# Kernel optimization log

Measured on AMD Instinct MI355X. Metric: run time of the kernel, lower is better.

Reference implementation:

```python
import jax, jax.numpy as jnp
import numpy as np

N_NODES = 50000
NEG_SLOPE = 0.01  # torch F.leaky_relu default


def setup_inputs() -> dict:
    key = jax.random.key(0)
    k1, k2, k3, k4, k5 = jax.random.split(key, 5)
    N, E, D = N_NODES, 800000, 128
    h = jax.random.normal(k1, (N, D), dtype=jnp.float32)
    src = jax.random.randint(k2, (E,), 0, N, dtype=jnp.int32)
    dst = jnp.sort(jax.random.randint(k3, (E,), 0, N, dtype=jnp.int32))
    # xavier-normal-ish scaling
    W_fc = jax.random.normal(k4, (D, D), dtype=jnp.float32) * np.sqrt(2.0 / (D + D))
    attn_w = jax.random.normal(k5, (1, 2 * D), dtype=jnp.float32) * np.sqrt(2.0 / (2 * D + 1))
    return {"h": h, "src": src, "dst": dst, "W_fc": W_fc, "attn_w": attn_w}


def reference(h, src, dst, W_fc, attn_w):
    N = h.shape[0]
    D = W_fc.shape[0]
    # node projection: z = fc(h)
    z = h @ W_fc.T                                   # [N, D]
    # edge attention: e = leaky_relu(attn_fc(cat(z_src, z_dst)))
    a_l, a_r = attn_w[0, :D], attn_w[0, D:]
    logits_l = z @ a_l                               # [N]
    logits_r = z @ a_r                               # [N]
    e = jax.nn.leaky_relu(logits_l[src] + logits_r[dst], NEG_SLOPE)  # [E]
    # segment softmax over incoming edges of each dst node
    m = jax.ops.segment_max(e, dst, num_segments=N)  # [N], -inf for empty
    m = jnp.where(jnp.isfinite(m), m, 0.0)
    ex = jnp.exp(e - m[dst])                         # [E]
    s = jax.ops.segment_sum(ex, dst, num_segments=N) # [N]
    alpha = ex / s[dst]                              # [E]
    # weighted neighbor aggregation: h_out[v] = sum_u alpha_uv * z_u
    out = jax.ops.segment_sum(alpha[:, None] * z[src], dst, num_segments=N)  # [N, D]
    return out
```

## Files before the change

kernel.cpp:

```cpp
#include <hip/hip_runtime.h>
#include <hip/hip_bf16.h>

#define DD 128
#define NEGS 0.01f

typedef float  f32x4 __attribute__((ext_vector_type(4)));
typedef __bf16 bf16x8 __attribute__((ext_vector_type(8)));
typedef unsigned short us8 __attribute__((ext_vector_type(8)));

__device__ __forceinline__ unsigned short f2bf(float f) {
    unsigned int u = __builtin_bit_cast(unsigned int, f);
    u += 0x7FFFu + ((u >> 16) & 1u);
    return (unsigned short)(u >> 16);
}
__device__ __forceinline__ float sb2f(unsigned int u, int byte) {
    return (float)(int)(signed char)((u >> (byte * 8)) & 0xffu);
}

__global__ __launch_bounds__(256)
void k_gemm(const float* __restrict__ h, const float* __restrict__ W,
            const float* __restrict__ attn, const int* __restrict__ dst,
            int E, int N, int NB,
            signed char* __restrict__ z8, float2* __restrict__ lls,
            float* __restrict__ lrv, int* __restrict__ start)
{
    if (blockIdx.x >= NB) {
        int n = (blockIdx.x - NB) * 256 + threadIdx.x;
        if (n > N) return;
        int lo = 0, hi = E;
        while (lo < hi) {
            int mid = (lo + hi) >> 1;
            if (dst[mid] < n) lo = mid + 1; else hi = mid;
        }
        start[n] = lo;
        return;
    }

    __shared__ unsigned short hs[128 * DD];
    __shared__ unsigned short ws[DD * DD];
    const int tid  = threadIdx.x;
    const int row0 = blockIdx.x * 128;

    {
        const int r = tid >> 4, c = tid & 15;
#pragma unroll
        for (int p = 0; p < DD; p += 16) {
            const int rr = p + r;
            const float* pw = W + (size_t)rr * DD + c * 8;
            float4 a = *(const float4*)pw, b = *(const float4*)(pw + 4);
            us8 v = { f2bf(a.x), f2bf(a.y), f2bf(a.z), f2bf(a.w),
                      f2bf(b.x), f2bf(b.y), f2bf(b.z), f2bf(b.w) };
            *(us8*)(ws + rr * DD + ((c ^ (rr & 15)) * 8)) = v;
        }
    }
    {
        const int r = tid >> 4, c = tid & 15;
#pragma unroll
        for (int p = 0; p < 128; p += 16) {
            const int rr = p + r;
            int gr = row0 + rr; if (gr > N - 1) gr = N - 1;
            const float* ph = h + (size_t)gr * DD + c * 8;
            float4 a = *(const float4*)ph, b = *(const float4*)(ph + 4);
            us8 v = { f2bf(a.x), f2bf(a.y), f2bf(a.z), f2bf(a.w),
                      f2bf(b.x), f2bf(b.y), f2bf(b.z), f2bf(b.w) };
            *(us8*)(hs + rr * DD + ((c ^ (rr & 15)) * 8)) = v;
        }
    }
    __syncthreads();

    const int w    = tid >> 6;
    const int lane = tid & 63;
    const int hl   = lane & 15;
    const int g    = lane >> 4;

    f32x4 acc[2][8];
#pragma unroll
    for (int rt = 0; rt < 2; ++rt)
#pragma unroll
        for (int jt = 0; jt < 8; ++jt) acc[rt][jt] = f32x4{0.f, 0.f, 0.f, 0.f};

#pragma unroll
    for (int kk = 0; kk < DD; kk += 32) {
        const int cb = (kk >> 3) + g;
        const int ra0 = w * 32 + hl;
        const int ra1 = ra0 + 16;
        bf16x8 a0 = *(const bf16x8*)(hs + ra0 * DD + ((cb ^ (ra0 & 15)) * 8));
        bf16x8 a1 = *(const bf16x8*)(hs + ra1 * DD + ((cb ^ (ra1 & 15)) * 8));
#pragma unroll
        for (int jt = 0; jt < 8; ++jt) {
            const int rb = jt * 16 + hl;
            bf16x8 b = *(const bf16x8*)(ws + rb * DD + ((cb ^ (rb & 15)) * 8));
            acc[0][jt] = __builtin_amdgcn_mfma_f32_16x16x32_bf16(a0, b, acc[0][jt], 0, 0, 0);
            acc[1][jt] = __builtin_amdgcn_mfma_f32_16x16x32_bf16(a1, b, acc[1][jt], 0, 0, 0);
        }
    }

    float aLc[8], aRc[8];
#pragma unroll
    for (int jt = 0; jt < 8; ++jt) {
        aLc[jt] = attn[jt * 16 + hl];
        aRc[jt] = attn[DD + jt * 16 + hl];
    }
#pragma unroll
    for (int rt = 0; rt < 2; ++rt) {
#pragma unroll
        for (int reg = 0; reg < 4; ++reg) {
            const int row = row0 + w * 32 + rt * 16 + g * 4 + reg;
            float pl = 0.f, pr = 0.f, am = 0.f;
#pragma unroll
            for (int jt = 0; jt < 8; ++jt) {
                float v = acc[rt][jt][reg];
                pl = fmaf(v, aLc[jt], pl);
                pr = fmaf(v, aRc[jt], pr);
                am = fmaxf(am, fabsf(v));
            }
#pragma unroll
            for (int o = 8; o >= 1; o >>= 1) {
                pl += __shfl_xor(pl, o);
                pr += __shfl_xor(pr, o);
                am = fmaxf(am, __shfl_xor(am, o));
            }
            if (row < N) {
                const float inv_s = (am > 0.f) ? 127.f / am : 0.f;
                if (hl == 0) {
                    lls[row] = make_float2(pl, am * (1.f / 127.f));
                    lrv[row] = pr;
                }
                signed char* zr = z8 + (size_t)row * DD;
#pragma unroll
                for (int jt = 0; jt < 8; ++jt)
                    zr[jt * 16 + hl] =
                        (signed char)__float2int_rn(acc[rt][jt][reg] * inv_s);
            }
        }
    }
}

__global__ __launch_bounds__(256)
void k_out(const signed char* __restrict__ z8, const int* __restrict__ src,
           const float2* __restrict__ lls, const float* __restrict__ lrv,
           const int* __restrict__ start, float* __restrict__ out, int N)
{
    int wid  = (blockIdx.x * 256 + threadIdx.x) >> 6;
    int lane = threadIdx.x & 63;
    if (wid >= N) return;
    const int s0 = start[wid], s1 = start[wid + 1];
    const int q = lane >> 4;
    const int c = lane & 15;
    const float lrn = lrv[wid];

    float acc[8];
#pragma unroll
    for (int k = 0; k < 8; ++k) acc[k] = 0.f;
    float ssum = 0.f;
    const int last = s1 - 1;

    for (int base = s0; base < s1; base += 8) {
        int t0 = base + q;
        int t1 = t0 + 4;
        int tc0 = (t0 <= last) ? t0 : last;
        int tc1 = (t1 <= last) ? t1 : last;
        int sj0 = __builtin_nontemporal_load(src + tc0);
        int sj1 = __builtin_nontemporal_load(src + tc1);
        float2 p0 = lls[sj0];
        float2 p1 = lls[sj1];
        float v0 = p0.x + lrn;  v0 = (v0 >= 0.f) ? v0 : NEGS * v0;
        float v1 = p1.x + lrn;  v1 = (v1 >= 0.f) ? v1 : NEGS * v1;
        float w0 = __expf(v0); if (t0 > last) w0 = 0.f;
        float w1 = __expf(v1); if (t1 > last) w1 = 0.f;
        uint2 z0 = *(const uint2*)(z8 + (size_t)sj0 * DD + c * 8);
        uint2 z1 = *(const uint2*)(z8 + (size_t)sj1 * DD + c * 8);
        ssum += w0 + w1;
        float u0 = w0 * p0.y;
        float u1 = w1 * p1.y;
        acc[0] = fmaf(u0, sb2f(z0.x, 0), fmaf(u1, sb2f(z1.x, 0), acc[0]));
        acc[1] = fmaf(u0, sb2f(z0.x, 1), fmaf(u1, sb2f(z1.x, 1), acc[1]));
        acc[2] = fmaf(u0, sb2f(z0.x, 2), fmaf(u1, sb2f(z1.x, 2), acc[2]));
        acc[3] = fmaf(u0, sb2f(z0.x, 3), fmaf(u1, sb2f(z1.x, 3), acc[3]));
        acc[4] = fmaf(u0, sb2f(z0.y, 0), fmaf(u1, sb2f(z1.y, 0), acc[4]));
        acc[5] = fmaf(u0, sb2f(z0.y, 1), fmaf(u1, sb2f(z1.y, 1), acc[5]));
        acc[6] = fmaf(u0, sb2f(z0.y, 2), fmaf(u1, sb2f(z1.y, 2), acc[6]));
        acc[7] = fmaf(u0, sb2f(z0.y, 3), fmaf(u1, sb2f(z1.y, 3), acc[7]));
    }
#pragma unroll
    for (int k = 0; k < 8; ++k) {
        acc[k] += __shfl_xor(acc[k], 16);
        acc[k] += __shfl_xor(acc[k], 32);
    }
    ssum += __shfl_xor(ssum, 16);
    ssum += __shfl_xor(ssum, 32);
    float inv = (s1 > s0) ? 1.0f / ssum : 0.f;

    float* orow = out + (size_t)wid * DD + c * 8;
    if (q == 0) {
        f32x4 o = {acc[0]*inv, acc[1]*inv, acc[2]*inv, acc[3]*inv};
        __builtin_nontemporal_store(o, (f32x4*)orow);
    } else if (q == 1) {
        f32x4 o = {acc[4]*inv, acc[5]*inv, acc[6]*inv, acc[7]*inv};
        __builtin_nontemporal_store(o, ((f32x4*)orow) + 1);
    }
}

extern "C" void kernel_launch(void* const* d_in, const int* in_sizes, int n_in,
                              void* d_out, int out_size, void* d_ws, size_t ws_size,
                              hipStream_t stream) {
    const float* h    = (const float*)d_in[0];
    const int*   src  = (const int*)d_in[1];
    const int*   dst  = (const int*)d_in[2];
    const float* W    = (const float*)d_in[3];
    const float* attn = (const float*)d_in[4];
    const int N = in_sizes[0] / DD;
    const int E = in_sizes[1];
    float* out = (float*)d_out;

    signed char* z8 = (signed char*)d_ws;
    float2* lls = (float2*)(z8 + (size_t)N * DD);
    float* lrv  = (float*)(lls + N);
    int* start  = (int*)(lrv + N);

    const int NB = (N + 127) / 128;
    const int SB = (N + 1 + 255) / 256;

    k_gemm<<<NB + SB, 256, 0, stream>>>(h, W, attn, dst, E, N, NB, z8, lls, lrv, start);
    k_out<<<(N + 3) / 4, 256, 0, stream>>>(z8, src, lls, lrv, start, out, N);
}
```

Baseline: 51.75 us.

## Split z8 into feature halves, precompute edge weights in separate kernel

Stores the int8 projected features as two 64-column halves and launches twice as many aggregation blocks, each covering one half of the feature dimension. This shrinks each gathered row segment so the half being gathered has a smaller cache footprint. A new per-edge kernel precomputes the exp weight and its scaled version into a workspace array, which removes the per-edge lls gather and exp from the aggregation loop. In exchange it adds a kernel launch, an extra E-sized write and read, and reads src and the edge weights twice.

```diff
diff --git a/kernel.cpp b/kernel.cpp
--- a/kernel.cpp
+++ b/kernel.cpp
@@ -5,6 +5,7 @@
 #define NEGS 0.01f
 
 typedef float  f32x4 __attribute__((ext_vector_type(4)));
+typedef float  f32x2 __attribute__((ext_vector_type(2)));
 typedef __bf16 bf16x8 __attribute__((ext_vector_type(8)));
 typedef unsigned short us8 __attribute__((ext_vector_type(8)));
 
@@ -101,6 +102,7 @@
         aLc[jt] = attn[jt * 16 + hl];
         aRc[jt] = attn[DD + jt * 16 + hl];
     }
+    const size_t halfStride = (size_t)N * 64;
 #pragma unroll
     for (int rt = 0; rt < 2; ++rt) {
 #pragma unroll
@@ -126,10 +128,10 @@
                     lls[row] = make_float2(pl, am * (1.f / 127.f));
                     lrv[row] = pr;
                 }
-                signed char* zr = z8 + (size_t)row * DD;
 #pragma unroll
                 for (int jt = 0; jt < 8; ++jt)
-                    zr[jt * 16 + hl] =
+                    z8[(size_t)(jt >> 2) * halfStride + (size_t)row * 64
+                       + (jt & 3) * 16 + hl] =
                         (signed char)__float2int_rn(acc[rt][jt][reg] * inv_s);
             }
         }
@@ -137,22 +139,36 @@
 }
 
 __global__ __launch_bounds__(256)
+void k_ew(const int* __restrict__ src, const int* __restrict__ dst,
+          const float2* __restrict__ lls, const float* __restrict__ lrv,
+          f32x2* __restrict__ pw, int E)
+{
+    int j = blockIdx.x * 256 + threadIdx.x;
+    if (j >= E) return;
+    float2 p = lls[src[j]];
+    float v = p.x + lrv[dst[j]];
+    float e = (v >= 0.f) ? v : NEGS * v;
+    float w = __expf(e);
+    f32x2 o = {w, w * p.y};
+    __builtin_nontemporal_store(o, pw + j);
+}
+
+__global__ __launch_bounds__(256)
 void k_out(const signed char* __restrict__ z8, const int* __restrict__ src,
-           const float2* __restrict__ lls, const float* __restrict__ lrv,
-           const int* __restrict__ start, float* __restrict__ out, int N)
+           const f32x2* __restrict__ pw, const int* __restrict__ start,
+           float* __restrict__ out, int N, int G2)
 {
-    int wid  = (blockIdx.x * 256 + threadIdx.x) >> 6;
+    const int half = (blockIdx.x >= G2) ? 1 : 0;
+    const int b    = blockIdx.x - half * G2;
+    int wid  = (b * 256 + threadIdx.x) >> 6;
     int lane = threadIdx.x & 63;
     if (wid >= N) return;
     const int s0 = start[wid], s1 = start[wid + 1];
     const int q = lane >> 4;
     const int c = lane & 15;
-    const float lrn = lrv[wid];
-
-    float acc[8];
-#pragma unroll
-    for (int k = 0; k < 8; ++k) acc[k] = 0.f;
-    float ssum = 0.f;
+    const signed char* zh = z8 + (size_t)half * N * 64;
+
+    float a0 = 0.f, a1 = 0.f, a2 = 0.f, a3 = 0.f, ssum = 0.f;
     const int last = s1 - 1;
 
     for (int base = s0; base < s1; base += 8) {
@@ -162,42 +178,32 @@
         int tc1 = (t1 <= last) ? t1 : last;
         int sj0 = __builtin_nontemporal_load(src + tc0);
         int sj1 = __builtin_nontemporal_load(src + tc1);
-        float2 p0 = lls[sj0];
-        float2 p1 = lls[sj1];
-        float v0 = p0.x + lrn;  v0 = (v0 >= 0.f) ? v0 : NEGS * v0;
-        float v1 = p1.x + lrn;  v1 = (v1 >= 0.f) ? v1 : NEGS * v1;
-        float w0 = __expf(v0); if (t0 > last) w0 = 0.f;
-        float w1 = __expf(v1); if (t1 > last) w1 = 0.f;
-        uint2 z0 = *(const uint2*)(z8 + (size_t)sj0 * DD + c * 8);
-        uint2 z1 = *(const uint2*)(z8 + (size_t)sj1 * DD + c * 8);
+        f32x2 p0 = __builtin_nontemporal_load(pw + tc0);
+        f32x2 p1 = __builtin_nontemporal_load(pw + tc1);
+        float w0 = p0[0], u0 = p0[1];
+        float w1 = p1[0], u1 = p1[1];
+        if (t0 > last) { w0 = 0.f; u0 = 0.f; }
+        if (t1 > last) { w1 = 0.f; u1 = 0.f; }
+        unsigned int z0 = *(const unsigned int*)(zh + (size_t)sj0 * 64 + c * 4);
+        unsigned int z1 = *(const unsigned int*)(zh + (size_t)sj1 * 64 + c * 4);
         ssum += w0 + w1;
-        float u0 = w0 * p0.y;
-        float u1 = w1 * p1.y;
-        acc[0] = fmaf(u0, sb2f(z0.x, 0), fmaf(u1, sb2f(z1.x, 0), acc[0]));
-        acc[1] = fmaf(u0, sb2f(z0.x, 1), fmaf(u1, sb2f(z1.x, 1), acc[1]));
-        acc[2] = fmaf(u0, sb2f(z0.x, 2), fmaf(u1, sb2f(z1.x, 2), acc[2]));
-        acc[3] = fmaf(u0, sb2f(z0.x, 3), fmaf(u1, sb2f(z1.x, 3), acc[3]));
-        acc[4] = fmaf(u0, sb2f(z0.y, 0), fmaf(u1, sb2f(z1.y, 0), acc[4]));
-        acc[5] = fmaf(u0, sb2f(z0.y, 1), fmaf(u1, sb2f(z1.y, 1), acc[5]));
-        acc[6] = fmaf(u0, sb2f(z0.y, 2), fmaf(u1, sb2f(z1.y, 2), acc[6]));
-        acc[7] = fmaf(u0, sb2f(z0.y, 3), fmaf(u1, sb2f(z1.y, 3), acc[7]));
-    }
-#pragma unroll
-    for (int k = 0; k < 8; ++k) {
-        acc[k] += __shfl_xor(acc[k], 16);
-        acc[k] += __shfl_xor(acc[k], 32);
-    }
+        a0 = fmaf(u0, sb2f(z0, 0), fmaf(u1, sb2f(z1, 0), a0));
+        a1 = fmaf(u0, sb2f(z0, 1), fmaf(u1, sb2f(z1, 1), a1));
+        a2 = fmaf(u0, sb2f(z0, 2), fmaf(u1, sb2f(z1, 2), a2));
+        a3 = fmaf(u0, sb2f(z0, 3), fmaf(u1, sb2f(z1, 3), a3));
+    }
+    a0 += __shfl_xor(a0, 16);  a0 += __shfl_xor(a0, 32);
+    a1 += __shfl_xor(a1, 16);  a1 += __shfl_xor(a1, 32);
+    a2 += __shfl_xor(a2, 16);  a2 += __shfl_xor(a2, 32);
+    a3 += __shfl_xor(a3, 16);  a3 += __shfl_xor(a3, 32);
     ssum += __shfl_xor(ssum, 16);
     ssum += __shfl_xor(ssum, 32);
     float inv = (s1 > s0) ? 1.0f / ssum : 0.f;
 
-    float* orow = out + (size_t)wid * DD + c * 8;
     if (q == 0) {
-        f32x4 o = {acc[0]*inv, acc[1]*inv, acc[2]*inv, acc[3]*inv};
-        __builtin_nontemporal_store(o, (f32x4*)orow);
-    } else if (q == 1) {
-        f32x4 o = {acc[4]*inv, acc[5]*inv, acc[6]*inv, acc[7]*inv};
-        __builtin_nontemporal_store(o, ((f32x4*)orow) + 1);
+        f32x4 o = {a0 * inv, a1 * inv, a2 * inv, a3 * inv};
+        __builtin_nontemporal_store(o,
+            (f32x4*)(out + (size_t)wid * DD + half * 64 + c * 4));
     }
 }
 
@@ -216,11 +222,14 @@
     signed char* z8 = (signed char*)d_ws;
     float2* lls = (float2*)(z8 + (size_t)N * DD);
     float* lrv  = (float*)(lls + N);
-    int* start  = (int*)(lrv + N);
+    f32x2* pw   = (f32x2*)(lrv + N);
+    int* start  = (int*)(pw + E);
 
     const int NB = (N + 127) / 128;
     const int SB = (N + 1 + 255) / 256;
+    const int G2 = (N + 3) / 4;
 
     k_gemm<<<NB + SB, 256, 0, stream>>>(h, W, attn, dst, E, N, NB, z8, lls, lrv, start);
-    k_out<<<(N + 3) / 4, 256, 0, stream>>>(z8, src, lls, lrv, start, out, N);
-}
+    k_ew<<<(E + 255) / 256, 256, 0, stream>>>(src, dst, lls, lrv, pw, E);
+    k_out<<<2 * G2, 256, 0, stream>>>(z8, src, pw, start, out, N, G2);
+}
```

Measured after the change: 79.69 us. 54.0% more time.
